# Kernel optimization log

Hardware: AMD Instinct MI355X
Metric: run time of the kernel (lower is better)

## Reference

```python
import jax, jax.numpy as jnp
import numpy as np

ETA = 1.0


def gcn_conv(x, W, b, src, dst, n_nodes):
    """PyG-style GCNConv: sym-normalized A+I propagation. x:[N,Fin] W:[Fin,Fout]."""
    h = x @ W  # [N, Fout]
    deg = jax.ops.segment_sum(jnp.ones(src.shape[0], h.dtype), dst, num_segments=n_nodes) + 1.0
    dinv = jax.lax.rsqrt(deg)  # deg includes self-loop
    norm = dinv[src] * dinv[dst]  # [E]
    agg = jax.ops.segment_sum(h[src] * norm[:, None], dst, num_segments=n_nodes)
    agg = agg + h * (dinv * dinv)[:, None]  # self-loop term, norm_ii = 1/deg_i
    return agg + b


def encode(x, edge_index, batch, num_graphs, W1, b1, W2, b2):
    n = x.shape[0]
    src, dst = edge_index[0], edge_index[1]
    z = jax.nn.relu(gcn_conv(x, W1, b1, src, dst, n))
    z = gcn_conv(z, W2, b2, src, dst, n)
    counts = jax.ops.segment_sum(jnp.ones(n, z.dtype), batch, num_segments=num_graphs)
    mean_p = jax.ops.segment_sum(z, batch, num_segments=num_graphs) / jnp.maximum(counts, 1.0)[:, None]
    max_p = jax.ops.segment_max(z, batch, num_segments=num_graphs)
    max_p = jnp.where(counts[:, None] > 0, max_p, 0.0)
    z_g = jnp.concatenate([mean_p, max_p], axis=1)  # [B, 2*out_dim]
    return z, z_g


def perturb(p, key, eta):
    sigma = jnp.maximum(jnp.std(p, ddof=1), 1e-6)
    return p + eta * sigma * jax.random.normal(key, p.shape, p.dtype)


def proj_head(g, P1w, P1b, P2w, P2b, P3w, P3b):
    h = jax.nn.relu(g @ P1w + P1b)
    h = jax.nn.relu(h @ P2w + P2b)
    return h @ P3w + P3b


def setup_inputs() -> dict:
    key = jax.random.key(0)
    ks = jax.random.split(key, 16)
    N, E, B = 50000, 400000, 64
    IN, HID, OUT = 128, 512, 256

    def glorot(k, fan_in, fan_out):
        s = jnp.sqrt(6.0 / (fan_in + fan_out))
        return jax.random.uniform(k, (fan_in, fan_out), jnp.float32, -s, s)

    x = jax.random.normal(ks[0], (N, IN), jnp.float32)
    edge_index = jax.random.randint(ks[1], (2, E), 0, N, jnp.int64)
    batch = jnp.sort(jax.random.randint(ks[2], (N,), 0, B, jnp.int64))
    return {
        "x": x, "edge_index": edge_index, "batch": batch, "num_graphs": B,
        "W1": glorot(ks[3], IN, HID), "b1": jnp.zeros((HID,), jnp.float32),
        "W2": glorot(ks[4], HID, OUT), "b2": jnp.zeros((OUT,), jnp.float32),
        "Wd": glorot(ks[5], OUT, IN), "bd": jnp.zeros((IN,), jnp.float32),
        "P1w": glorot(ks[6], 2 * OUT, 256), "P1b": jnp.zeros((256,), jnp.float32),
        "P2w": glorot(ks[7], 256, 128), "P2b": jnp.zeros((128,), jnp.float32),
        "P3w": glorot(ks[8], 128, 64), "P3b": jnp.zeros((64,), jnp.float32),
    }


def reference(x, edge_index, batch, num_graphs, W1, b1, W2, b2, Wd, bd,
              P1w, P1b, P2w, P2b, P3w, P3b):
    n = x.shape[0]
    src, dst = edge_index[0], edge_index[1]

    # clean branch
    z_node, z_g = encode(x, edge_index, batch, num_graphs, W1, b1, W2, b2)
    x_hat = gcn_conv(z_node, Wd, bd, src, dst, n)

    # perturbed encoder (SimGRACE-style weight noise)
    nk = jax.random.split(jax.random.key(42), 4)
    W1h = perturb(W1, nk[0], ETA)
    b1h = perturb(b1, nk[1], ETA)
    W2h = perturb(W2, nk[2], ETA)
    b2h = perturb(b2, nk[3], ETA)
    zhat_node, zhat_g = encode(x, edge_index, batch, num_graphs, W1h, b1h, W2h, b2h)

    h_g = proj_head(z_g, P1w, P1b, P2w, P2b, P3w, P3b)
    hhat_g = proj_head(zhat_g, P1w, P1b, P2w, P2b, P3w, P3b)
    return (z_node, z_g, zhat_node, zhat_g, h_g, hhat_g, x_hat)
```

## Files before the change

### kernel.cpp

```cpp
#include <hip/hip_runtime.h>

typedef unsigned short u16;
typedef unsigned int u32;
typedef short bf16x8 __attribute__((ext_vector_type(8)));
typedef float f32x4 __attribute__((ext_vector_type(4)));

__host__ __device__ inline u32 rotl32(u32 x, int r) { return (x << r) | (x >> (32 - r)); }

__host__ __device__ inline void tf_r4(u32& x0, u32& x1, int r0, int r1, int r2, int r3) {
  x0 += x1; x1 = rotl32(x1, r0); x1 ^= x0;
  x0 += x1; x1 = rotl32(x1, r1); x1 ^= x0;
  x0 += x1; x1 = rotl32(x1, r2); x1 ^= x0;
  x0 += x1; x1 = rotl32(x1, r3); x1 ^= x0;
}

__host__ __device__ inline void tf2x32(u32 k0, u32 k1, u32 c0, u32 c1, u32* o0, u32* o1) {
  u32 ks2 = 0x1BD11BDAu ^ k0 ^ k1;
  u32 x0 = c0 + k0, x1 = c1 + k1;
  tf_r4(x0, x1, 13, 15, 26, 6);  x0 += k1;  x1 += ks2 + 1u;
  tf_r4(x0, x1, 17, 29, 16, 24); x0 += ks2; x1 += k0 + 2u;
  tf_r4(x0, x1, 13, 15, 26, 6);  x0 += k0;  x1 += k1 + 3u;
  tf_r4(x0, x1, 17, 29, 16, 24); x0 += k1;  x1 += ks2 + 4u;
  tf_r4(x0, x1, 13, 15, 26, 6);  x0 += ks2; x1 += k0 + 5u;
  *o0 = x0; *o1 = x1;
}

__device__ inline float erfinv_f(float x) {
  float w = -log1pf(-x * x);
  float p;
  if (w < 5.0f) {
    w -= 2.5f;
    p = 2.81022636e-08f;
    p = 3.43273939e-07f + p * w;
    p = -3.5233877e-06f + p * w;
    p = -4.39150654e-06f + p * w;
    p = 0.00021858087f + p * w;
    p = -0.00125372503f + p * w;
    p = -0.00417768164f + p * w;
    p = 0.246640727f + p * w;
    p = 1.50140941f + p * w;
  } else {
    w = sqrtf(w) - 3.0f;
    p = -0.000200214257f;
    p = 0.000100950558f + p * w;
    p = 0.00134934322f + p * w;
    p = -0.00367342844f + p * w;
    p = 0.00573950773f + p * w;
    p = -0.0076224613f + p * w;
    p = 0.00943887047f + p * w;
    p = 1.00167406f + p * w;
    p = 2.83297682f + p * w;
  }
  return p * x;
}

__device__ inline float bits2normal(u32 b) {
  float f = __uint_as_float((b >> 9) | 0x3F800000u) - 1.0f;
  float u = f * 2.0f - 0.99999994f;
  u = fmaxf(u, -0.99999994f);
  return 1.41421356f * erfinv_f(u);
}

__device__ inline void stor(u16* p, float v) {
  u32 x = __float_as_uint(v);
  *p = (u16)((x + 0x7FFFu + ((x >> 16) & 1u)) >> 16);
}
__device__ inline u16 f2b(float v) {
  u32 x = __float_as_uint(v);
  return (u16)((x + 0x7FFFu + ((x >> 16) & 1u)) >> 16);
}
__device__ inline float blo(u32 w) { return __uint_as_float(w << 16); }
__device__ inline float bhi(u32 w) { return __uint_as_float(w & 0xFFFF0000u); }

__global__ __launch_bounds__(256) void k_prepA(const int* __restrict__ ei, int* __restrict__ cnt, int E,
                                               const float* __restrict__ W1, const float* __restrict__ b1,
                                               const float* __restrict__ W2, const float* __restrict__ b2,
                                               double* __restrict__ psd,
                                               const float* __restrict__ Wd,
                                               u16* __restrict__ W1T, u16* __restrict__ W2T, u16* __restrict__ WdT,
                                               const float* __restrict__ x, u16* __restrict__ xb,
                                               int N, int c1) {
  __shared__ double sh[256];
  __shared__ double sh2[256];
  int b = blockIdx.x;
  if (b < c1) {
    int e = b * 256 + threadIdx.x;
    if (e < E) atomicAdd(&cnt[ei[E + e]], 1);
    return;
  }
  b -= c1;
  if (b < 64) {
    int t = b >> 4, ch = b & 15;
    const float* p; int n;
    if (t == 0) { p = W1; n = 128 * 512; }
    else if (t == 1) { p = b1; n = 512; }
    else if (t == 2) { p = W2; n = 512 * 256; }
    else { p = b2; n = 256; }
    int s0 = (int)((long long)n * ch / 16), s1 = (int)((long long)n * (ch + 1) / 16);
    double s = 0.0, ss = 0.0;
    for (int i = s0 + threadIdx.x; i < s1; i += 256) { double v = p[i]; s += v; ss += v * v; }
    sh[threadIdx.x] = s; sh2[threadIdx.x] = ss;
    __syncthreads();
    for (int o = 128; o > 0; o >>= 1) {
      if (threadIdx.x < o) { sh[threadIdx.x] += sh[threadIdx.x + o]; sh2[threadIdx.x] += sh2[threadIdx.x + o]; }
      __syncthreads();
    }
    if (threadIdx.x == 0) { psd[b * 2] = sh[0]; psd[b * 2 + 1] = sh2[0]; }
    return;
  }
  b -= 64;
  if (b < 256) {
    int j = b * 256 + threadIdx.x;
    int k = j >> 9, n = j & 511;
    W1T[(size_t)n * 128 + k] = f2b(W1[j]);
    return;
  }
  b -= 256;
  if (b < 512) {
    int j = b * 256 + threadIdx.x;
    int k = j >> 8, n = j & 255;
    W2T[(size_t)n * 512 + k] = f2b(W2[j]);
    return;
  }
  b -= 512;
  if (b < 128) {
    int j = b * 256 + threadIdx.x;
    int k = j >> 7, n = j & 127;
    WdT[(size_t)n * 256 + k] = f2b(Wd[j]);
    return;
  }
  b -= 128;
  {
    int j = b * 256 + threadIdx.x;
    int n4 = N * 128 / 4;
    if (j < n4) {
      float4 v = ((const float4*)x)[j];
      ((u32*)xb)[j * 2] = ((u32)f2b(v.x)) | (((u32)f2b(v.y)) << 16);
      ((u32*)xb)[j * 2 + 1] = ((u32)f2b(v.z)) | (((u32)f2b(v.w)) << 16);
    }
  }
}

__global__ __launch_bounds__(1024) void k_scan_local(const int* __restrict__ cnt,
                                                     int* __restrict__ incl, int* __restrict__ bsum,
                                                     int n) {
  __shared__ int buf[1024];
  int i = blockIdx.x * 1024 + threadIdx.x;
  int v = (i < n) ? cnt[i] : 0;
  buf[threadIdx.x] = v;
  __syncthreads();
  for (int off = 1; off < 1024; off <<= 1) {
    int t = (threadIdx.x >= off) ? buf[threadIdx.x - off] : 0;
    __syncthreads();
    buf[threadIdx.x] += t;
    __syncthreads();
  }
  if (i < n) incl[i] = buf[threadIdx.x];
  if (threadIdx.x == 1023) bsum[blockIdx.x] = buf[1023];
}

__global__ __launch_bounds__(256) void k_small2(int* __restrict__ bsum, int nb,
                                                const double* __restrict__ psd, float* __restrict__ sigma) {
  if (blockIdx.x == 0) {
    __shared__ int buf[256];
    int v = (threadIdx.x < nb) ? bsum[threadIdx.x] : 0;
    buf[threadIdx.x] = v;
    __syncthreads();
    for (int off = 1; off < 256; off <<= 1) {
      int t = (threadIdx.x >= off) ? buf[threadIdx.x - off] : 0;
      __syncthreads();
      buf[threadIdx.x] += t;
      __syncthreads();
    }
    if (threadIdx.x < nb) bsum[threadIdx.x] = buf[threadIdx.x] - v;
  } else {
    int l = threadIdx.x;
    if (l < 64) {
      double s = psd[l * 2], ss = psd[l * 2 + 1];
      for (int off = 1; off < 16; off <<= 1) { s += __shfl_xor(s, off); ss += __shfl_xor(ss, off); }
      if ((l & 15) == 0) {
        int t = l >> 4;
        int n = (t == 0) ? 128 * 512 : (t == 1) ? 512 : (t == 2) ? 512 * 256 : 256;
        double mean = s / n;
        double var = (ss - s * mean) / (double)(n - 1);
        if (var < 0.0) var = 0.0;
        sigma[t] = fmaxf((float)sqrt(var), 1e-6f);
      }
    }
  }
}

__global__ __launch_bounds__(1024) void k_scan_final(const int* __restrict__ cnt,
                                                     const int* __restrict__ incl,
                                                     const int* __restrict__ bsum,
                                                     int* __restrict__ row_ptr, int* __restrict__ cursor,
                                                     float* __restrict__ dinv, int n, int E) {
  int i = blockIdx.x * 1024 + threadIdx.x;
  if (i < n) {
    int c = cnt[i];
    int ex = incl[i] + bsum[blockIdx.x] - c;
    row_ptr[i] = ex;
    cursor[i] = ex;
    dinv[i] = 1.0f / sqrtf((float)(c + 1));
  }
  if (i == 0) row_ptr[n] = E;
}

__global__ void k_place(const int* __restrict__ ei, int* __restrict__ cursor,
                        const float* __restrict__ dinv, int* __restrict__ src_sorted,
                        float* __restrict__ w_sorted, int E) {
  int e = blockIdx.x * blockDim.x + threadIdx.x;
  if (e < E) {
    int s = ei[e], d = ei[E + e];
    int slot = atomicAdd(&cursor[d], 1);
    src_sorted[slot] = s;
    w_sorted[slot] = dinv[s] * dinv[d];
  }
}

__global__ __launch_bounds__(256) void k_pxper(const float* __restrict__ W1, const float* __restrict__ b1,
                                               const float* __restrict__ W2, const float* __restrict__ b2,
                                               u16* __restrict__ W1hT, float* __restrict__ b1h,
                                               u16* __restrict__ W2hT, float* __restrict__ b2h,
                                               float* __restrict__ bcat,
                                               const float* __restrict__ sigma,
                                               u32 k00, u32 k01, u32 k10, u32 k11,
                                               u32 k20, u32 k21, u32 k30, u32 k31,
                                               const u16* __restrict__ xb, u16* __restrict__ px,
                                               const int* __restrict__ rp, const int* __restrict__ src,
                                               const float* __restrict__ wst, const float* __restrict__ dinv,
                                               int n) {
  int b = blockIdx.x;
  u32 r0, r1;
  if (b < 256) {
    int j = b * 256 + threadIdx.x;
    tf2x32(k00, k01, 0u, (u32)j, &r0, &r1);
    float v = W1[j] + sigma[0] * bits2normal(r0 ^ r1);
    int k = j >> 9, nn = j & 511;
    W1hT[(size_t)nn * 128 + k] = f2b(v);
    return;
  }
  b -= 256;
  if (b < 2) {
    int j = b * 256 + threadIdx.x;
    tf2x32(k10, k11, 0u, (u32)j, &r0, &r1);
    b1h[j] = b1[j] + sigma[1] * bits2normal(r0 ^ r1);
    return;
  }
  b -= 2;
  if (b < 512) {
    int j = b * 256 + threadIdx.x;
    tf2x32(k20, k21, 0u, (u32)j, &r0, &r1);
    float v = W2[j] + sigma[2] * bits2normal(r0 ^ r1);
    int k = j >> 8, nn = j & 255;
    W2hT[(size_t)nn * 512 + k] = f2b(v);
    return;
  }
  b -= 512;
  if (b < 1) {
    int j = threadIdx.x;
    tf2x32(k30, k31, 0u, (u32)j, &r0, &r1);
    float v = b2[j] + sigma[3] * bits2normal(r0 ^ r1);
    b2h[j] = v;
    bcat[256 + j] = v;
    bcat[j] = b2[j];
    return;
  }
  b -= 1;
  int wv = threadIdx.x >> 6, lane = threadIdx.x & 63;
  int node = b * 4 + wv;
  if (node >= n) return;
  float a0 = 0.f, a1 = 0.f;
  int s0 = rp[node], s1 = rp[node + 1];
  int s = s0;
  for (; s + 8 <= s1; s += 8) {
    u32 v[8]; float wg[8];
#pragma unroll
    for (int u = 0; u < 8; ++u) {
      int r = src[s + u];
      wg[u] = wst[s + u];
      v[u] = *((const u32*)(xb + (size_t)r * 128) + lane);
    }
#pragma unroll
    for (int u = 0; u < 8; ++u) { a0 += wg[u] * blo(v[u]); a1 += wg[u] * bhi(v[u]); }
  }
  for (; s < s1; ++s) {
    float wgt = wst[s];
    int r = src[s];
    u32 w = *((const u32*)(xb + (size_t)r * 128) + lane);
    a0 += wgt * blo(w); a1 += wgt * bhi(w);
  }
  float sw = dinv[node]; sw *= sw;
  u32 w = *((const u32*)(xb + (size_t)node * 128) + lane);
  a0 += sw * blo(w); a1 += sw * bhi(w);
  u32 o = ((u32)f2b(a0)) | (((u32)f2b(a1)) << 16);
  *((u32*)(px + (size_t)node * 128) + lane) = o;
}

template <bool RELU, bool BIAS>
__device__ inline void mgemm_tile(u16* lds_all, const u16* __restrict__ A, const u16* __restrict__ BT,
                                  const float* __restrict__ bias, u16* __restrict__ C,
                                  int M, int N, int K, int ldc, int coloff, int bx, int by) {
  u16* As = lds_all;
  u16* Bs = lds_all + 8192;
  const int t = threadIdx.x;
  const int w = t >> 6, lane = t & 63;
  const int brow = by * 128;
  const int bcol = bx * 128;
  const int wr = w >> 1, wc = w & 1;

  f32x4 acc[4][4];
#pragma unroll
  for (int m = 0; m < 4; ++m)
#pragma unroll
    for (int n = 0; n < 4; ++n) acc[m][n] = (f32x4){0.f, 0.f, 0.f, 0.f};

  for (int kt = 0; kt < K; kt += 64) {
#pragma unroll
    for (int j = 0; j < 4; ++j) {
      int c = j * 4 + w;
      int li = c * 64 + lane;
      int row = li >> 3, col8 = li & 7;
      int col8s = col8 ^ (row & 7);
      int ar = brow + row; if (ar > M - 1) ar = M - 1;
      __builtin_amdgcn_global_load_lds(
          (const __attribute__((address_space(1))) void*)(A + (size_t)ar * K + kt + col8s * 8),
          (__attribute__((address_space(3))) void*)(As + c * 512), 16, 0, 0);
      __builtin_amdgcn_global_load_lds(
          (const __attribute__((address_space(1))) void*)(BT + (size_t)(bcol + row) * K + kt + col8s * 8),
          (__attribute__((address_space(3))) void*)(Bs + c * 512), 16, 0, 0);
    }
    __syncthreads();
    bf16x8 af[4][2], bb[4][2];
#pragma unroll
    for (int kk = 0; kk < 2; ++kk) {
      int ch = kk * 4 + (lane >> 4);
      int chs = ch ^ (lane & 7);
#pragma unroll
      for (int m = 0; m < 4; ++m)
        af[m][kk] = *(const bf16x8*)(As + (wr * 64 + m * 16 + (lane & 15)) * 64 + chs * 8);
#pragma unroll
      for (int n = 0; n < 4; ++n)
        bb[n][kk] = *(const bf16x8*)(Bs + (wc * 64 + n * 16 + (lane & 15)) * 64 + chs * 8);
    }
#pragma unroll
    for (int kk = 0; kk < 2; ++kk)
#pragma unroll
      for (int m = 0; m < 4; ++m)
#pragma unroll
        for (int n = 0; n < 4; ++n)
          acc[m][n] = __builtin_amdgcn_mfma_f32_16x16x32_bf16(af[m][kk], bb[n][kk], acc[m][n], 0, 0, 0);
    __syncthreads();
  }

  u16* wlds = lds_all + w * 4096;
#pragma unroll
  for (int m = 0; m < 4; ++m) {
    int lr0 = m * 16 + (lane >> 4) * 4;
#pragma unroll
    for (int n = 0; n < 4; ++n) {
      int lc = n * 16 + (lane & 15);
      float bv = BIAS ? bias[bcol + wc * 64 + lc] : 0.0f;
      int chunk = lc >> 3, wi = lc & 7;
#pragma unroll
      for (int q = 0; q < 4; ++q) {
        int lr = lr0 + q;
        float v = acc[m][n][q] + bv;
        if (RELU) v = fmaxf(v, 0.0f);
        wlds[lr * 64 + ((chunk ^ (lr & 7)) << 3) + wi] = f2b(v);
      }
    }
  }
  int sr = lane >> 3;
  int sc = lane & 7;
#pragma unroll
  for (int i = 0; i < 8; ++i) {
    int lr = i * 8 + sr;
    int gr = brow + wr * 64 + lr;
    if (gr < M) {
      uint4 vv = *(const uint4*)(wlds + lr * 64 + ((sc ^ (lr & 7)) << 3));
      *(uint4*)(C + (size_t)gr * ldc + coloff + bcol + wc * 64 + sc * 8) = vv;
    }
  }
}

template <bool RELU, bool BIAS>
__global__ __launch_bounds__(256) void k_mgemm2(const u16* A0, const u16* A1,
                                                const u16* BT0, const u16* BT1,
                                                const float* bias0, const float* bias1,
                                                u16* C0, u16* C1,
                                                int M, int N, int K, int ldc, int co0, int co1) {
  __shared__ u16 lds_all[16384];
  int z = blockIdx.z;
  mgemm_tile<RELU, BIAS>(lds_all, z ? A1 : A0, z ? BT1 : BT0, z ? bias1 : bias0,
                         z ? C1 : C0, M, N, K, ldc, z ? co1 : co0, blockIdx.x, blockIdx.y);
}

__global__ __launch_bounds__(256) void k_mgemm1(const u16* __restrict__ A, const u16* __restrict__ BT,
                                                u16* __restrict__ C, int M) {
  __shared__ u16 lds_all[16384];
  mgemm_tile<false, false>(lds_all, A, BT, nullptr, C, M, 128, 256, 128, 0, 0, blockIdx.x);
}

__global__ __launch_bounds__(256) void k_agg512(const u16* __restrict__ ycat,
                                                float* __restrict__ zc, u16* __restrict__ zcb,
                                                float* __restrict__ zh,
                                                const int* __restrict__ rp, const int* __restrict__ src,
                                                const float* __restrict__ wst, const float* __restrict__ dinv,
                                                const float* __restrict__ bcat, int n) {
  int wv = threadIdx.x >> 6, lane = threadIdx.x & 63;
  int node = blockIdx.x * 4 + wv;
  if (node >= n) return;
  float acc[8] = {};
  int s0 = rp[node], s1 = rp[node + 1];
  int s = s0;
  for (; s + 4 <= s1; s += 4) {
    uint4 v[4]; float wg[4];
#pragma unroll
    for (int u = 0; u < 4; ++u) {
      int r = src[s + u];
      wg[u] = wst[s + u];
      v[u] = *((const uint4*)(ycat + (size_t)r * 512) + lane);
    }
#pragma unroll
    for (int u = 0; u < 4; ++u)
#pragma unroll
      for (int q = 0; q < 4; ++q) {
        u32 word = ((const u32*)&v[u])[q];
        acc[2 * q]     += wg[u] * blo(word);
        acc[2 * q + 1] += wg[u] * bhi(word);
      }
  }
  for (; s < s1; ++s) {
    float wgt = wst[s];
    int r = src[s];
    uint4 v = *((const uint4*)(ycat + (size_t)r * 512) + lane);
#pragma unroll
    for (int q = 0; q < 4; ++q) {
      u32 word = ((const u32*)&v)[q];
      acc[2 * q]     += wgt * blo(word);
      acc[2 * q + 1] += wgt * bhi(word);
    }
  }
  float sw = dinv[node]; sw *= sw;
  uint4 v = *((const uint4*)(ycat + (size_t)node * 512) + lane);
#pragma unroll
  for (int q = 0; q < 4; ++q) {
    u32 word = ((const u32*)&v)[q];
    acc[2 * q]     += sw * blo(word);
    acc[2 * q + 1] += sw * bhi(word);
  }
  int f0 = lane * 8;
#pragma unroll
  for (int j = 0; j < 8; ++j) acc[j] += bcat[f0 + j];
  if (lane < 32) {
    float* o = zc + (size_t)node * 256 + f0;
    u16* ob = zcb + (size_t)node * 256 + f0;
#pragma unroll
    for (int j = 0; j < 8; ++j) { o[j] = acc[j]; ob[j] = f2b(acc[j]); }
  } else {
    float* o = zh + (size_t)node * 256 + (f0 - 256);
#pragma unroll
    for (int j = 0; j < 8; ++j) o[j] = acc[j];
  }
}

__device__ inline int lbound(const int* a, int n, int v) {
  int lo = 0, hi = n;
  while (lo < hi) { int mid = (lo + hi) >> 1; if (a[mid] < v) lo = mid + 1; else hi = mid; }
  return lo;
}

#define POOL_NCH 32

__global__ __launch_bounds__(256) void k_poolpart2(const float* __restrict__ zc,
                                                   const float* __restrict__ zh,
                                                   const int* __restrict__ batch,
                                                   float* __restrict__ psum, float* __restrict__ pmax,
                                                   int n) {
  int g = blockIdx.x, yy = blockIdx.y;
  int half = (yy >= POOL_NCH) ? 1 : 0;
  int ch = yy - half * POOL_NCH;
  const float* z = half ? zh : zc;
  __shared__ int ss, se;
  if (threadIdx.x == 0) { ss = lbound(batch, n, g); se = lbound(batch, n, g + 1); }
  __syncthreads();
  int start = ss, len = se - ss;
  int c0 = start + (int)((long long)len * ch / POOL_NCH);
  int c1 = start + (int)((long long)len * (ch + 1) / POOL_NCH);
  int f = threadIdx.x;
  float acc = 0.0f, mx = -INFINITY;
  for (int i = c0; i < c1; ++i) {
    float v = z[(size_t)i * 256 + f];
    acc += v;
    mx = fmaxf(mx, v);
  }
  size_t o = ((size_t)(half * 64 + g) * POOL_NCH + ch) * 256 + f;
  psum[o] = acc;
  pmax[o] = mx;
}

__global__ __launch_bounds__(256) void k_finaldec(const u16* __restrict__ yd, float* __restrict__ xhat,
                                                  const int* __restrict__ rp, const int* __restrict__ src,
                                                  const float* __restrict__ wst, const float* __restrict__ dinv,
                                                  const float* __restrict__ bd, int n, int ab,
                                                  const float* __restrict__ psum, const float* __restrict__ pmax,
                                                  const int* __restrict__ batch,
                                                  float* __restrict__ z_g, float* __restrict__ zhat_g,
                                                  float* __restrict__ gcat) {
  if (blockIdx.x < ab) {
    int wv = threadIdx.x >> 6, lane = threadIdx.x & 63;
    int node = blockIdx.x * 4 + wv;
    if (node >= n) return;
    float a0 = 0.f, a1 = 0.f;
    int s0 = rp[node], s1 = rp[node + 1];
    int s = s0;
    for (; s + 8 <= s1; s += 8) {
      u32 v[8]; float wg[8];
#pragma unroll
      for (int u = 0; u < 8; ++u) {
        int r = src[s + u];
        wg[u] = wst[s + u];
        v[u] = *((const u32*)(yd + (size_t)r * 128) + lane);
      }
#pragma unroll
      for (int u = 0; u < 8; ++u) { a0 += wg[u] * blo(v[u]); a1 += wg[u] * bhi(v[u]); }
    }
    for (; s < s1; ++s) {
      float wgt = wst[s];
      int r = src[s];
      u32 w = *((const u32*)(yd + (size_t)r * 128) + lane);
      a0 += wgt * blo(w); a1 += wgt * bhi(w);
    }
    float sw = dinv[node]; sw *= sw;
    u32 w = *((const u32*)(yd + (size_t)node * 128) + lane);
    a0 += sw * blo(w); a1 += sw * bhi(w);
    float2 o;
    o.x = a0 + bd[lane * 2];
    o.y = a1 + bd[lane * 2 + 1];
    *((float2*)(xhat + (size_t)node * 128) + lane) = o;
    return;
  }
  int gg = blockIdx.x - ab, f = threadIdx.x;
  int g = gg & 63, half = gg >> 6;
  float s = 0.0f, m = -INFINITY;
#pragma unroll 4
  for (int c = 0; c < POOL_NCH; ++c) {
    size_t o = ((size_t)gg * POOL_NCH + c) * 256 + f;
    s += psum[o];
    m = fmaxf(m, pmax[o]);
  }
  __shared__ int ss, se;
  if (threadIdx.x == 0) { ss = lbound(batch, n, g); se = lbound(batch, n, g + 1); }
  __syncthreads();
  int cnt = se - ss;
  float mean = s / fmaxf((float)cnt, 1.0f);
  float mxo = (cnt > 0) ? m : 0.0f;
  float* zg = half ? zhat_g : z_g;
  zg[(size_t)g * 512 + f] = mean;
  zg[(size_t)g * 512 + 256 + f] = mxo;
  gcat[(size_t)gg * 512 + f] = mean;
  gcat[(size_t)gg * 512 + 256 + f] = mxo;
}

__global__ __launch_bounds__(256) void k_proj(const float* __restrict__ gcat,
                                              const float* __restrict__ P1w, const float* __restrict__ P1b,
                                              const float* __restrict__ P2w, const float* __restrict__ P2b,
                                              const float* __restrict__ P3w, const float* __restrict__ P3b,
                                              float* __restrict__ outg) {
  __shared__ float gi[512];
  __shared__ float h1[256];
  __shared__ float h2[128];
  int r = blockIdx.x;
  int t = threadIdx.x;
  gi[t] = gcat[(size_t)r * 512 + t];
  gi[t + 256] = gcat[(size_t)r * 512 + 256 + t];
  __syncthreads();
  float a = 0.f;
#pragma unroll 8
  for (int k = 0; k < 512; ++k) a += gi[k] * P1w[k * 256 + t];
  h1[t] = fmaxf(a + P1b[t], 0.f);
  __syncthreads();
  if (t < 128) {
    float a2 = 0.f;
#pragma unroll 8
    for (int k = 0; k < 256; ++k) a2 += h1[k] * P2w[k * 128 + t];
    h2[t] = fmaxf(a2 + P2b[t], 0.f);
  }
  __syncthreads();
  if (t < 64) {
    float a3 = 0.f;
#pragma unroll 8
    for (int k = 0; k < 128; ++k) a3 += h2[k] * P3w[k * 64 + t];
    outg[(size_t)r * 64 + t] = a3 + P3b[t];
  }
}

extern "C" void kernel_launch(void* const* d_in, const int* in_sizes, int n_in,
                              void* d_out, int out_size, void* d_ws, size_t ws_size,
                              hipStream_t stream) {
  const float* x   = (const float*)d_in[0];
  const int*   ei  = (const int*)d_in[1];
  const int*   bat = (const int*)d_in[2];
  const float* W1  = (const float*)d_in[4];
  const float* b1  = (const float*)d_in[5];
  const float* W2  = (const float*)d_in[6];
  const float* b2  = (const float*)d_in[7];
  const float* Wd  = (const float*)d_in[8];
  const float* bd  = (const float*)d_in[9];
  const float* P1w = (const float*)d_in[10];
  const float* P1b = (const float*)d_in[11];
  const float* P2w = (const float*)d_in[12];
  const float* P2b = (const float*)d_in[13];
  const float* P3w = (const float*)d_in[14];
  const float* P3b = (const float*)d_in[15];

  const int N = in_sizes[0] / 128;
  const int E = in_sizes[1] / 2;
  const int B = 64;
  const int NB = (N + 1023) / 1024;

  char* w = (char*)d_ws;
  auto carve = [&](size_t bytes) -> void* {
    void* p = (void*)w;
    w += (bytes + 255) & ~(size_t)255;
    return p;
  };
  int*    cnt        = (int*)carve((size_t)N * 4);
  int*    row_ptr    = (int*)carve((size_t)(N + 1) * 4);
  int*    cursor     = (int*)carve((size_t)N * 4);
  float*  dinv       = (float*)carve((size_t)N * 4);
  int*    incl       = (int*)carve((size_t)N * 4);
  int*    bsum       = (int*)carve((size_t)1024 * 4);
  int*    src_sorted = (int*)carve((size_t)E * 4);
  float*  w_sorted   = (float*)carve((size_t)E * 4);
  float*  sigma      = (float*)carve(256);
  double* psd        = (double*)carve((size_t)64 * 2 * 8);
  float*  b1h        = (float*)carve((size_t)512 * 4);
  float*  b2h        = (float*)carve((size_t)256 * 4);
  float*  bcat       = (float*)carve((size_t)512 * 4);
  u16*    W1T        = (u16*)carve((size_t)128 * 512 * 2);
  u16*    W2T        = (u16*)carve((size_t)512 * 256 * 2);
  u16*    WdT        = (u16*)carve((size_t)256 * 128 * 2);
  u16*    W1hT       = (u16*)carve((size_t)128 * 512 * 2);
  u16*    W2hT       = (u16*)carve((size_t)512 * 256 * 2);
  u16*    xb         = (u16*)carve((size_t)N * 128 * 2);
  u16*    px         = (u16*)carve((size_t)N * 128 * 2);
  u16*    z1c        = (u16*)carve((size_t)N * 512 * 2);
  u16*    z1p        = (u16*)carve((size_t)N * 512 * 2);
  u16*    ycat       = (u16*)carve((size_t)N * 512 * 2);
  u16*    znb        = (u16*)carve((size_t)N * 256 * 2);
  float*  gcat       = (float*)carve((size_t)128 * 512 * 4);
  float*  psum       = (float*)carve((size_t)2 * B * POOL_NCH * 256 * 4);
  float*  pmax       = (float*)carve((size_t)2 * B * POOL_NCH * 256 * 4);
  u16*    yd         = ycat;

  float* out       = (float*)d_out;
  float* z_node    = out;
  float* z_g       = z_node + (size_t)N * 256;
  float* zhat_node = z_g + (size_t)B * 512;
  float* zhat_g    = zhat_node + (size_t)N * 256;
  float* h_g       = zhat_g + (size_t)B * 512;
  float* x_hat     = h_g + (size_t)2 * B * 64;

  u32 nk[4][2];
  for (u32 i = 0; i < 4; ++i) tf2x32(0u, 42u, 0u, i, &nk[i][0], &nk[i][1]);

  const int c1 = (E + 255) / 256;
  const int n4b = (N * 128 / 4 + 255) / 256;
  const int prepABlocks = c1 + 64 + 256 + 512 + 128 + n4b;
  const int aggBlocks = (N + 3) / 4;
  const int MB = (N + 127) / 128;

  hipMemsetAsync(cnt, 0, (size_t)N * 4, stream);
  k_prepA<<<prepABlocks, 256, 0, stream>>>(ei, cnt, E, W1, b1, W2, b2, psd,
                                           Wd, W1T, W2T, WdT, x, xb, N, c1);
  k_scan_local<<<NB, 1024, 0, stream>>>(cnt, incl, bsum, N);
  k_small2<<<2, 256, 0, stream>>>(bsum, NB, psd, sigma);
  k_scan_final<<<NB, 1024, 0, stream>>>(cnt, incl, bsum, row_ptr, cursor, dinv, N, E);
  k_place<<<(E + 255) / 256, 256, 0, stream>>>(ei, cursor, dinv, src_sorted, w_sorted, E);

  k_pxper<<<771 + aggBlocks, 256, 0, stream>>>(W1, b1, W2, b2, W1hT, b1h, W2hT, b2h, bcat, sigma,
                                               nk[0][0], nk[0][1], nk[1][0], nk[1][1],
                                               nk[2][0], nk[2][1], nk[3][0], nk[3][1],
                                               xb, px, row_ptr, src_sorted, w_sorted, dinv, N);

  k_mgemm2<true, true><<<dim3(4, MB, 2), 256, 0, stream>>>(px, px, W1T, W1hT, b1, b1h,
                                                           z1c, z1p, N, 512, 128, 512, 0, 0);
  k_mgemm2<false, false><<<dim3(2, MB, 2), 256, 0, stream>>>(z1c, z1p, W2T, W2hT, nullptr, nullptr,
                                                             ycat, ycat, N, 256, 512, 512, 0, 256);

  k_agg512<<<aggBlocks, 256, 0, stream>>>(ycat, z_node, znb, zhat_node,
                                          row_ptr, src_sorted, w_sorted, dinv, bcat, N);

  k_mgemm1<<<MB, 256, 0, stream>>>(znb, WdT, yd, N);
  dim3 pgrid(B, 2 * POOL_NCH);
  k_poolpart2<<<pgrid, 256, 0, stream>>>(z_node, zhat_node, bat, psum, pmax, N);

  k_finaldec<<<aggBlocks + 128, 256, 0, stream>>>(yd, x_hat, row_ptr, src_sorted, w_sorted, dinv, bd,
                                                  N, aggBlocks, psum, pmax, bat, z_g, zhat_g, gcat);

  k_proj<<<128, 256, 0, stream>>>(gcat, P1w, P1b, P2w, P2b, P3w, P3b, h_g);
}
```

Before: 469.9 us.

## Add layer-1 GEMM kernel reusing A tile across all output column blocks

Replaces the generic layer-1 GEMM launch (4 column-blocks per row tile) with a dedicated kernel that loads the full K=128 A row tile into LDS once and loops over the four 128-wide output column blocks, streaming only the weight tiles. This cuts redundant reads of the propagated input and launches fewer blocks. It uses 64KB of LDS per block and serializes the column blocks, so occupancy and parallelism drop. The generic GEMM also gets a launch-bounds occupancy hint of 4 blocks.

Result: no change. 471.2 us (+0.3%).

```diff
diff --git a/kernel.cpp b/kernel.cpp
--- a/kernel.cpp
+++ b/kernel.cpp
@@ -297,6 +297,107 @@
   *((u32*)(px + (size_t)node * 128) + lane) = o;
 }
 
+__global__ __launch_bounds__(256) void k_mgemmL1(const u16* __restrict__ A,
+                                                 const u16* __restrict__ BT0, const u16* __restrict__ BT1,
+                                                 const float* __restrict__ bias0, const float* __restrict__ bias1,
+                                                 u16* __restrict__ C0, u16* __restrict__ C1,
+                                                 int M) {
+  __shared__ u16 As[16384];
+  __shared__ u16 Bs[16384];
+  const u16* BT = blockIdx.y ? BT1 : BT0;
+  const float* bias = blockIdx.y ? bias1 : bias0;
+  u16* C = blockIdx.y ? C1 : C0;
+  const int t = threadIdx.x;
+  const int w = t >> 6, lane = t & 63;
+  const int brow = blockIdx.x * 128;
+  const int wr = w >> 1, wc = w & 1;
+
+#pragma unroll
+  for (int j = 0; j < 8; ++j) {
+    int c = j * 4 + w;
+    int lc = c * 64 + lane;
+    int row = lc >> 4, ch = lc & 15;
+    int chs = ch ^ (row & 15);
+    int ar = brow + row; if (ar > M - 1) ar = M - 1;
+    __builtin_amdgcn_global_load_lds(
+        (const __attribute__((address_space(1))) void*)(A + (size_t)ar * 128 + chs * 8),
+        (__attribute__((address_space(3))) void*)(As + c * 512), 16, 0, 0);
+  }
+
+  for (int cb = 0; cb < 4; ++cb) {
+    int bcol = cb * 128;
+#pragma unroll
+    for (int j = 0; j < 8; ++j) {
+      int c = j * 4 + w;
+      int lc = c * 64 + lane;
+      int row = lc >> 4, ch = lc & 15;
+      int chs = ch ^ (row & 15);
+      __builtin_amdgcn_global_load_lds(
+          (const __attribute__((address_space(1))) void*)(BT + (size_t)(bcol + row) * 128 + chs * 8),
+          (__attribute__((address_space(3))) void*)(Bs + c * 512), 16, 0, 0);
+    }
+    __syncthreads();
+
+    f32x4 acc[4][4];
+#pragma unroll
+    for (int m = 0; m < 4; ++m)
+#pragma unroll
+      for (int n = 0; n < 4; ++n) acc[m][n] = (f32x4){0.f, 0.f, 0.f, 0.f};
+
+#pragma unroll
+    for (int kk = 0; kk < 4; ++kk) {
+      int ch = kk * 2 + (lane >> 5);
+      ch = kk * 4 + (lane >> 4);
+      bf16x8 af[4], bb[4];
+#pragma unroll
+      for (int m = 0; m < 4; ++m) {
+        int row = wr * 64 + m * 16 + (lane & 15);
+        af[m] = *(const bf16x8*)(As + row * 128 + ((ch ^ (row & 15)) << 3));
+      }
+#pragma unroll
+      for (int n = 0; n < 4; ++n) {
+        int row = wc * 64 + n * 16 + (lane & 15);
+        bb[n] = *(const bf16x8*)(Bs + row * 128 + ((ch ^ (row & 15)) << 3));
+      }
+#pragma unroll
+      for (int m = 0; m < 4; ++m)
+#pragma unroll
+        for (int n = 0; n < 4; ++n)
+          acc[m][n] = __builtin_amdgcn_mfma_f32_16x16x32_bf16(af[m], bb[n], acc[m][n], 0, 0, 0);
+    }
+    __syncthreads();
+
+    u16* wlds = Bs + w * 4096;
+#pragma unroll
+    for (int m = 0; m < 4; ++m) {
+      int lr0 = m * 16 + (lane >> 4) * 4;
+#pragma unroll
+      for (int n = 0; n < 4; ++n) {
+        int lc = n * 16 + (lane & 15);
+        float bv = bias[bcol + wc * 64 + lc];
+        int chunk = lc >> 3, wi = lc & 7;
+#pragma unroll
+        for (int q = 0; q < 4; ++q) {
+          int lr = lr0 + q;
+          float v = fmaxf(acc[m][n][q] + bv, 0.0f);
+          wlds[lr * 64 + ((chunk ^ (lr & 7)) << 3) + wi] = f2b(v);
+        }
+      }
+    }
+    int sr = lane >> 3, sc = lane & 7;
+#pragma unroll
+    for (int i = 0; i < 8; ++i) {
+      int lr = i * 8 + sr;
+      int gr = brow + wr * 64 + lr;
+      if (gr < M) {
+        uint4 vv = *(const uint4*)(wlds + lr * 64 + ((sc ^ (lr & 7)) << 3));
+        *(uint4*)(C + (size_t)gr * 512 + bcol + wc * 64 + sc * 8) = vv;
+      }
+    }
+    __syncthreads();
+  }
+}
+
 template <bool RELU, bool BIAS>
 __device__ inline void mgemm_tile(u16* lds_all, const u16* __restrict__ A, const u16* __restrict__ BT,
                                   const float* __restrict__ bias, u16* __restrict__ C,
@@ -371,8 +472,7 @@
       }
     }
   }
-  int sr = lane >> 3;
-  int sc = lane & 7;
+  int sr = lane >> 3, sc = lane & 7;
 #pragma unroll
   for (int i = 0; i < 8; ++i) {
     int lr = i * 8 + sr;
@@ -385,11 +485,11 @@
 }
 
 template <bool RELU, bool BIAS>
-__global__ __launch_bounds__(256) void k_mgemm2(const u16* A0, const u16* A1,
-                                                const u16* BT0, const u16* BT1,
-                                                const float* bias0, const float* bias1,
-                                                u16* C0, u16* C1,
-                                                int M, int N, int K, int ldc, int co0, int co1) {
+__global__ __launch_bounds__(256, 4) void k_mgemm2(const u16* A0, const u16* A1,
+                                                   const u16* BT0, const u16* BT1,
+                                                   const float* bias0, const float* bias1,
+                                                   u16* C0, u16* C1,
+                                                   int M, int N, int K, int ldc, int co0, int co1) {
   __shared__ u16 lds_all[16384];
   int z = blockIdx.z;
   mgemm_tile<RELU, BIAS>(lds_all, z ? A1 : A0, z ? BT1 : BT0, z ? bias1 : bias0,
@@ -685,8 +785,8 @@
                                                nk[2][0], nk[2][1], nk[3][0], nk[3][1],
                                                xb, px, row_ptr, src_sorted, w_sorted, dinv, N);
 
-  k_mgemm2<true, true><<<dim3(4, MB, 2), 256, 0, stream>>>(px, px, W1T, W1hT, b1, b1h,
-                                                           z1c, z1p, N, 512, 128, 512, 0, 0);
+  k_mgemmL1<<<dim3(MB, 2), 256, 0, stream>>>(px, W1T, W1hT, b1, b1h, z1c, z1p, N);
+
   k_mgemm2<false, false><<<dim3(2, MB, 2), 256, 0, stream>>>(z1c, z1p, W2T, W2hT, nullptr, nullptr,
                                                              ycat, ycat, N, 256, 512, 512, 0, 256);
 
```
